# Optimization experiments

Measured on AMD Instinct MI355X. Metric: run time of the kernel, lower is better.

## Reference

```python
import jax, jax.numpy as jnp
import numpy as np

N_MODELS = 16
IN_F = 1024
OUT_F = 1024
N_TOK = 8192


def setup_inputs() -> dict:
    key = jax.random.key(0)
    k1, k2, k3, k4 = jax.random.split(key, 4)
    x = jax.random.normal(k1, (N_TOK, IN_F), dtype=jnp.float32)
    idxs = jax.random.randint(k2, (N_TOK,), 0, N_MODELS, dtype=jnp.int64)
    w = jax.random.normal(k3, (N_MODELS, IN_F, OUT_F), dtype=jnp.float32) * 0.02
    b = jax.random.normal(k4, (N_MODELS, OUT_F), dtype=jnp.float32) * 0.02
    return {"x": x, "idxs": idxs, "w": w, "b": b}


def reference(x, idxs, w, b):
    # Equivalent math to the torch loop: for each expert i, tokens with
    # idxs==i get x @ w[i] + b[i]; finally ReLU over all outputs.
    # Loop over the small fixed expert count; selection by mask avoids
    # materializing the [N, E, out] tensor or gathering per-token weights.
    y = jnp.zeros((x.shape[0], w.shape[2]), dtype=x.dtype)
    for i in range(w.shape[0]):
        yi = x @ w[i] + b[i]  # [N, out]
        y = jnp.where((idxs == i)[:, None], yi, y)
    return jax.nn.relu(y)
```

## Files before the change

### kernel.cpp

```cpp
#include <hip/hip_runtime.h>
#include <hip/hip_bf16.h>
#include <stdint.h>

#define N_MODELS 16
#define IN_F 1024
#define OUT_F 1024
#define N_TOK 8192
#define MAX_MT 80

typedef unsigned short u16;
using us4   = __attribute__((ext_vector_type(4))) unsigned short;
using s16x8 = __attribute__((ext_vector_type(8))) short;
using f32x4 = __attribute__((ext_vector_type(4))) float;

__device__ __forceinline__ u16 f2bf(float f) {
    union { float f; uint32_t u; } v;
    v.f = f;
    uint32_t u = v.u;
    u += 0x7fffu + ((u >> 16) & 1u);
    return (u16)(u >> 16);
}

__device__ __forceinline__ void gload16(const u16* g, u16* l) {
    __builtin_amdgcn_global_load_lds(
        (const __attribute__((address_space(1))) void*)g,
        (__attribute__((address_space(3))) void*)l, 16, 0, 0);
}

#define ROW 17
__global__ __launch_bounds__(256)
void setup_kernel(const int* __restrict__ idxs,
                  int* __restrict__ perm,
                  int* __restrict__ offs,
                  int* __restrict__ tile_off)
{
    __shared__ int cnt[256 * ROW];
    __shared__ int offsS[N_MODELS + 1];
    int t = threadIdx.x;

#pragma unroll
    for (int e = 0; e < N_MODELS; ++e) cnt[t * ROW + e] = 0;
    __syncthreads();

    int base = t * 32;
#pragma unroll
    for (int i = 0; i < 32; ++i) {
        int e = idxs[base + i];
        cnt[t * ROW + e] += 1;
    }
    __syncthreads();

#pragma unroll
    for (int s = 1; s < 256; s <<= 1) {
        int v[N_MODELS];
#pragma unroll
        for (int e = 0; e < N_MODELS; ++e)
            v[e] = (t >= s) ? cnt[(t - s) * ROW + e] : 0;
        __syncthreads();
#pragma unroll
        for (int e = 0; e < N_MODELS; ++e)
            cnt[t * ROW + e] += v[e];
        __syncthreads();
    }

    if (t == 0) {
        int o = 0, to = 0;
        for (int e = 0; e < N_MODELS; ++e) {
            int c = cnt[255 * ROW + e];
            offsS[e] = o;
            offs[e] = o; tile_off[e] = to;
            to += (c + 127) >> 7;
            o  += c;
        }
        offsS[N_MODELS] = o;
        offs[N_MODELS] = o; tile_off[N_MODELS] = to;
    }
    __syncthreads();

    int cur[N_MODELS];
#pragma unroll
    for (int e = 0; e < N_MODELS; ++e)
        cur[e] = offsS[e] + ((t > 0) ? cnt[(t - 1) * ROW + e] : 0);
    __syncthreads();
#pragma unroll
    for (int e = 0; e < N_MODELS; ++e) cnt[t * ROW + e] = cur[e];

#pragma unroll
    for (int i = 0; i < 32; ++i) {
        int tok = base + i;
        int e = idxs[tok];
        int p = cnt[t * ROW + e]++;
        perm[p] = tok;
    }
}

#define WBLOCKS (16 * 8 * 16)
#define XBLOCKS (MAX_MT * 8)

__global__ __launch_bounds__(256)
void prep_kernel(const float* __restrict__ w, const float* __restrict__ x,
                 const int* __restrict__ perm, const int* __restrict__ offs,
                 const int* __restrict__ tile_off,
                 u16* __restrict__ wT, u16* __restrict__ xg)
{
    int t  = threadIdx.x;
    int bx = blockIdx.x;

    if (bx < WBLOCKS) {
        int e   = bx >> 7;
        int nt  = (bx >> 4) & 7;
        int kb2 = bx & 15;
        const float* wp = w + (size_t)e * (IN_F * OUT_F) + (size_t)kb2 * 64 * OUT_F + nt * 128;
        u16* ob = wT + ((size_t)(e * 8 + nt) * 32 + kb2 * 2) * 4096;
        int n    = t & 127;
        int half = t >> 7;
#pragma unroll
        for (int i = 0; i < 4; ++i) {
            int ko = half + i * 2;
            s16x8 v;
#pragma unroll
            for (int j = 0; j < 8; ++j)
                v[j] = (short)f2bf(wp[(size_t)(ko * 8 + j) * OUT_F + n]);
            *(s16x8*)(ob + ((size_t)((ko >> 2) * 4 + (ko & 3)) * 128 + n) * 8) = v;
        }
    } else {
        __shared__ u16 sh[4096];
        int bx2 = bx - WBLOCKS;
        int mt  = bx2 >> 3;
        int kg  = bx2 & 7;
        int total = tile_off[N_MODELS];
        if (mt >= total) return;
        int e = 0;
        while (tile_off[e + 1] <= mt) ++e;
        int s0   = offs[e] + (mt - tile_off[e]) * 128;
        int sEnd = offs[e + 1];
        int r0   = t >> 3;
        int apos = t & 7;
        int toks[4];
#pragma unroll
        for (int i = 0; i < 4; ++i) {
            int r = r0 + i * 32;
            toks[i] = (s0 + r < sEnd) ? perm[s0 + r] : -1;
        }
        u16* outx = xg + (size_t)mt * 32 * 4096;
        for (int kb4 = 0; kb4 < 4; ++kb4) {
            int kb = kg * 4 + kb4;
#pragma unroll
            for (int i = 0; i < 4; ++i) {
                int r = r0 + i * 32;
                int k = kb * 32 + apos * 4;
                float4 v;
                if (toks[i] >= 0) v = *(const float4*)(x + (size_t)toks[i] * IN_F + k);
                else              v = make_float4(0.f, 0.f, 0.f, 0.f);
                us4 pk; pk.x = f2bf(v.x); pk.y = f2bf(v.y); pk.z = f2bf(v.z); pk.w = f2bf(v.w);
                *(us4*)(&sh[(apos >> 1) * 1024 + r * 8 + (apos & 1) * 4]) = pk;
            }
            __syncthreads();
#pragma unroll
            for (int i = 0; i < 2; ++i) {
                int c = t + i * 256;
                *(s16x8*)(outx + (size_t)kb * 4096 + c * 8) = *(const s16x8*)(&sh[c * 8]);
            }
            __syncthreads();
        }
    }
}

__global__ __launch_bounds__(256)
void gemm_kernel(const u16* __restrict__ xg, const u16* __restrict__ wT,
                 const float* __restrict__ bias,
                 const int* __restrict__ perm, const int* __restrict__ offs,
                 const int* __restrict__ tile_off,
                 float* __restrict__ out)
{
    __shared__ u16 As[4096];
    __shared__ u16 Bs[4096];
    __shared__ int   permS[128];
    __shared__ float biasS[128];
    __shared__ int   toS[N_MODELS + 1];

    int t  = threadIdx.x;
    int bt = blockIdx.y;
    int nt = blockIdx.x;

    if (t <= N_MODELS) toS[t] = tile_off[t];
    __syncthreads();
    if (bt >= toS[N_MODELS]) return;

    int e = 0;
    while (toS[e + 1] <= bt) ++e;
    int s0   = offs[e] + (bt - toS[e]) * 128;
    int sEnd = offs[e + 1];
    int mValid = sEnd - s0; if (mValid > 128) mValid = 128;

    if (t < 128) {
        permS[t] = (s0 + t < sEnd) ? perm[s0 + t] : 0;
        biasS[t] = bias[(size_t)e * OUT_F + nt * 128 + t];
    }

    const u16* atile = xg + (size_t)bt * 32 * 4096;
    const u16* btile = wT + ((size_t)(e * 8 + nt) * 32) * 4096;

    int lane = t & 63;
    int wv   = t >> 6;
    int wm   = (wv >> 1) * 64;
    int wn   = (wv & 1) * 64;
    int m    = lane & 15;
    int q    = lane >> 4;

    f32x4 acc[4][4];
#pragma unroll
    for (int i = 0; i < 4; ++i)
#pragma unroll
        for (int j = 0; j < 4; ++j)
            acc[i][j] = (f32x4){0.f, 0.f, 0.f, 0.f};

    int c = wv * 2;

    for (int kb = 0; kb < 32; ++kb) {
        const u16* ga = atile + kb * 4096;
        const u16* gb = btile + kb * 4096;
        gload16(ga + (c    ) * 512 + lane * 8, &As[(c    ) * 512]);
        gload16(ga + (c + 1) * 512 + lane * 8, &As[(c + 1) * 512]);
        gload16(gb + (c    ) * 512 + lane * 8, &Bs[(c    ) * 512]);
        gload16(gb + (c + 1) * 512 + lane * 8, &Bs[(c + 1) * 512]);
        __syncthreads();

        s16x8 af[4], bf[4];
#pragma unroll
        for (int mt2 = 0; mt2 < 4; ++mt2)
            af[mt2] = *(const s16x8*)(&As[q * 1024 + (wm + mt2 * 16 + m) * 8]);
#pragma unroll
        for (int nt2 = 0; nt2 < 4; ++nt2)
            bf[nt2] = *(const s16x8*)(&Bs[q * 1024 + (wn + nt2 * 16 + m) * 8]);
#pragma unroll
        for (int mt2 = 0; mt2 < 4; ++mt2)
#pragma unroll
            for (int nt2 = 0; nt2 < 4; ++nt2)
                acc[mt2][nt2] = __builtin_amdgcn_mfma_f32_16x16x32_bf16(
                    af[mt2], bf[nt2], acc[mt2][nt2], 0, 0, 0);
        __syncthreads();
    }

#pragma unroll
    for (int mt2 = 0; mt2 < 4; ++mt2) {
        int rbase = wm + mt2 * 16 + q * 4;
#pragma unroll
        for (int i = 0; i < 4; ++i) {
            int r = rbase + i;
            if (r < mValid) {
                int tok = permS[r];
                float* orow = out + (size_t)tok * OUT_F + nt * 128;
#pragma unroll
                for (int nt2 = 0; nt2 < 4; ++nt2) {
                    int col = wn + nt2 * 16 + m;
                    float v = acc[mt2][nt2][i] + biasS[col];
                    orow[col] = v > 0.f ? v : 0.f;
                }
            }
        }
    }
}

extern "C" void kernel_launch(void* const* d_in, const int* in_sizes, int n_in,
                              void* d_out, int out_size, void* d_ws, size_t ws_size,
                              hipStream_t stream) {
    const float* x    = (const float*)d_in[0];
    const int*   idxs = (const int*)d_in[1];
    const float* w    = (const float*)d_in[2];
    const float* b    = (const float*)d_in[3];
    float* out = (float*)d_out;

    u16* wT = (u16*)d_ws;
    u16* xg = wT + (size_t)N_MODELS * IN_F * OUT_F;
    int* perm     = (int*)(xg + (size_t)MAX_MT * 32 * 4096);
    int* offs     = perm + N_TOK;
    int* tile_off = offs + (N_MODELS + 1);

    setup_kernel<<<1, 256, 0, stream>>>(idxs, perm, offs, tile_off);
    prep_kernel<<<WBLOCKS + XBLOCKS, 256, 0, stream>>>(w, x, perm, offs, tile_off, wT, xg);
    gemm_kernel<<<dim3(8, MAX_MT), 256, 0, stream>>>(xg, wT, b, perm, offs, tile_off, out);
}
```

Baseline: 186.3 us.

## Fuse token gather and bf16 conversion into GEMM, merge routing into weight prep

Removes the separate x gather/convert pass and its intermediate bf16 buffer. The GEMM now loads fp32 rows of x directly through the permutation and converts them to bf16 in LDS each k-step. The routing setup becomes one extra block of the weight-conversion kernel, dropping a launch. In exchange, the GEMM re-reads fp32 x once per N-tile (8x) through uncoalesced, synchronous loads instead of async global-to-LDS copies.

```diff
diff --git a/kernel.cpp b/kernel.cpp
--- a/kernel.cpp
+++ b/kernel.cpp
@@ -27,82 +27,16 @@
         (__attribute__((address_space(3))) void*)l, 16, 0, 0);
 }
 
+#define WBLOCKS (16 * 8 * 16)
 #define ROW 17
+
 __global__ __launch_bounds__(256)
-void setup_kernel(const int* __restrict__ idxs,
-                  int* __restrict__ perm,
-                  int* __restrict__ offs,
-                  int* __restrict__ tile_off)
+void prep_kernel(const float* __restrict__ w, const int* __restrict__ idxs,
+                 u16* __restrict__ wT,
+                 int* __restrict__ perm, int* __restrict__ offs,
+                 int* __restrict__ tile_off)
 {
-    __shared__ int cnt[256 * ROW];
-    __shared__ int offsS[N_MODELS + 1];
-    int t = threadIdx.x;
-
-#pragma unroll
-    for (int e = 0; e < N_MODELS; ++e) cnt[t * ROW + e] = 0;
-    __syncthreads();
-
-    int base = t * 32;
-#pragma unroll
-    for (int i = 0; i < 32; ++i) {
-        int e = idxs[base + i];
-        cnt[t * ROW + e] += 1;
-    }
-    __syncthreads();
-
-#pragma unroll
-    for (int s = 1; s < 256; s <<= 1) {
-        int v[N_MODELS];
-#pragma unroll
-        for (int e = 0; e < N_MODELS; ++e)
-            v[e] = (t >= s) ? cnt[(t - s) * ROW + e] : 0;
-        __syncthreads();
-#pragma unroll
-        for (int e = 0; e < N_MODELS; ++e)
-            cnt[t * ROW + e] += v[e];
-        __syncthreads();
-    }
-
-    if (t == 0) {
-        int o = 0, to = 0;
-        for (int e = 0; e < N_MODELS; ++e) {
-            int c = cnt[255 * ROW + e];
-            offsS[e] = o;
-            offs[e] = o; tile_off[e] = to;
-            to += (c + 127) >> 7;
-            o  += c;
-        }
-        offsS[N_MODELS] = o;
-        offs[N_MODELS] = o; tile_off[N_MODELS] = to;
-    }
-    __syncthreads();
-
-    int cur[N_MODELS];
-#pragma unroll
-    for (int e = 0; e < N_MODELS; ++e)
-        cur[e] = offsS[e] + ((t > 0) ? cnt[(t - 1) * ROW + e] : 0);
-    __syncthreads();
-#pragma unroll
-    for (int e = 0; e < N_MODELS; ++e) cnt[t * ROW + e] = cur[e];
-
-#pragma unroll
-    for (int i = 0; i < 32; ++i) {
-        int tok = base + i;
-        int e = idxs[tok];
-        int p = cnt[t * ROW + e]++;
-        perm[p] = tok;
-    }
-}
-
-#define WBLOCKS (16 * 8 * 16)
-#define XBLOCKS (MAX_MT * 8)
-
-__global__ __launch_bounds__(256)
-void prep_kernel(const float* __restrict__ w, const float* __restrict__ x,
-                 const int* __restrict__ perm, const int* __restrict__ offs,
-                 const int* __restrict__ tile_off,
-                 u16* __restrict__ wT, u16* __restrict__ xg)
-{
+    __shared__ int shmem[256 * ROW + N_MODELS + 1];
     int t  = threadIdx.x;
     int bx = blockIdx.x;
 
@@ -110,64 +44,79 @@
         int e   = bx >> 7;
         int nt  = (bx >> 4) & 7;
         int kb2 = bx & 15;
-        const float* wp = w + (size_t)e * (IN_F * OUT_F) + (size_t)kb2 * 64 * OUT_F + nt * 128;
-        u16* ob = wT + ((size_t)(e * 8 + nt) * 32 + kb2 * 2) * 4096;
         int n    = t & 127;
         int half = t >> 7;
+        const float* wp = w + (size_t)e * (IN_F * OUT_F) + (size_t)kb2 * 64 * OUT_F + nt * 128 + n;
+        u16* ob = wT + ((size_t)(e * 8 + nt) * 32 + kb2 * 2) * 4096;
+        float r[32];
+#pragma unroll
+        for (int i = 0; i < 4; ++i) {
+            int ko = half + i * 2;
+#pragma unroll
+            for (int j = 0; j < 8; ++j)
+                r[i * 8 + j] = wp[(size_t)(ko * 8 + j) * OUT_F];
+        }
 #pragma unroll
         for (int i = 0; i < 4; ++i) {
             int ko = half + i * 2;
             s16x8 v;
 #pragma unroll
-            for (int j = 0; j < 8; ++j)
-                v[j] = (short)f2bf(wp[(size_t)(ko * 8 + j) * OUT_F + n]);
+            for (int j = 0; j < 8; ++j) v[j] = (short)f2bf(r[i * 8 + j]);
             *(s16x8*)(ob + ((size_t)((ko >> 2) * 4 + (ko & 3)) * 128 + n) * 8) = v;
         }
     } else {
-        __shared__ u16 sh[4096];
-        int bx2 = bx - WBLOCKS;
-        int mt  = bx2 >> 3;
-        int kg  = bx2 & 7;
-        int total = tile_off[N_MODELS];
-        if (mt >= total) return;
-        int e = 0;
-        while (tile_off[e + 1] <= mt) ++e;
-        int s0   = offs[e] + (mt - tile_off[e]) * 128;
-        int sEnd = offs[e + 1];
-        int r0   = t >> 3;
-        int apos = t & 7;
-        int toks[4];
-#pragma unroll
-        for (int i = 0; i < 4; ++i) {
-            int r = r0 + i * 32;
-            toks[i] = (s0 + r < sEnd) ? perm[s0 + r] : -1;
-        }
-        u16* outx = xg + (size_t)mt * 32 * 4096;
-        for (int kb4 = 0; kb4 < 4; ++kb4) {
-            int kb = kg * 4 + kb4;
-#pragma unroll
-            for (int i = 0; i < 4; ++i) {
-                int r = r0 + i * 32;
-                int k = kb * 32 + apos * 4;
-                float4 v;
-                if (toks[i] >= 0) v = *(const float4*)(x + (size_t)toks[i] * IN_F + k);
-                else              v = make_float4(0.f, 0.f, 0.f, 0.f);
-                us4 pk; pk.x = f2bf(v.x); pk.y = f2bf(v.y); pk.z = f2bf(v.z); pk.w = f2bf(v.w);
-                *(us4*)(&sh[(apos >> 1) * 1024 + r * 8 + (apos & 1) * 4]) = pk;
+        int* cnt   = shmem;
+        int* offsS = shmem + 256 * ROW;
+#pragma unroll
+        for (int e = 0; e < N_MODELS; ++e) cnt[t * ROW + e] = 0;
+        __syncthreads();
+        int base = t * 32;
+#pragma unroll
+        for (int i = 0; i < 32; ++i) cnt[t * ROW + idxs[base + i]] += 1;
+        __syncthreads();
+#pragma unroll
+        for (int s = 1; s < 256; s <<= 1) {
+            int v[N_MODELS];
+#pragma unroll
+            for (int e = 0; e < N_MODELS; ++e)
+                v[e] = (t >= s) ? cnt[(t - s) * ROW + e] : 0;
+            __syncthreads();
+#pragma unroll
+            for (int e = 0; e < N_MODELS; ++e)
+                cnt[t * ROW + e] += v[e];
+            __syncthreads();
+        }
+        if (t == 0) {
+            int o = 0, to = 0;
+            for (int e = 0; e < N_MODELS; ++e) {
+                int c = cnt[255 * ROW + e];
+                offsS[e] = o;
+                offs[e] = o; tile_off[e] = to;
+                to += (c + 127) >> 7;
+                o  += c;
             }
-            __syncthreads();
-#pragma unroll
-            for (int i = 0; i < 2; ++i) {
-                int c = t + i * 256;
-                *(s16x8*)(outx + (size_t)kb * 4096 + c * 8) = *(const s16x8*)(&sh[c * 8]);
-            }
-            __syncthreads();
+            offsS[N_MODELS] = o;
+            offs[N_MODELS] = o; tile_off[N_MODELS] = to;
+        }
+        __syncthreads();
+        int cur[N_MODELS];
+#pragma unroll
+        for (int e = 0; e < N_MODELS; ++e)
+            cur[e] = offsS[e] + ((t > 0) ? cnt[(t - 1) * ROW + e] : 0);
+        __syncthreads();
+#pragma unroll
+        for (int e = 0; e < N_MODELS; ++e) cnt[t * ROW + e] = cur[e];
+#pragma unroll
+        for (int i = 0; i < 32; ++i) {
+            int tok = base + i;
+            int e = idxs[tok];
+            perm[cnt[t * ROW + e]++] = tok;
         }
     }
 }
 
 __global__ __launch_bounds__(256)
-void gemm_kernel(const u16* __restrict__ xg, const u16* __restrict__ wT,
+void gemm_kernel(const float* __restrict__ x, const u16* __restrict__ wT,
                  const float* __restrict__ bias,
                  const int* __restrict__ perm, const int* __restrict__ offs,
                  const int* __restrict__ tile_off,
@@ -197,8 +146,19 @@
         permS[t] = (s0 + t < sEnd) ? perm[s0 + t] : 0;
         biasS[t] = bias[(size_t)e * OUT_F + nt * 128 + t];
     }
-
-    const u16* atile = xg + (size_t)bt * 32 * 4096;
+    __syncthreads();
+
+    const float* px[4];
+    int la[4];
+#pragma unroll
+    for (int i = 0; i < 4; ++i) {
+        int c    = t + i * 256;
+        int r    = c >> 3;
+        int apos = c & 7;
+        px[i] = x + (size_t)permS[r] * IN_F + apos * 4;
+        la[i] = (apos >> 1) * 1024 + r * 8 + (apos & 1) * 4;
+    }
+
     const u16* btile = wT + ((size_t)(e * 8 + nt) * 32) * 4096;
 
     int lane = t & 63;
@@ -215,15 +175,22 @@
         for (int j = 0; j < 4; ++j)
             acc[i][j] = (f32x4){0.f, 0.f, 0.f, 0.f};
 
-    int c = wv * 2;
+    int c2 = wv * 2;
 
     for (int kb = 0; kb < 32; ++kb) {
-        const u16* ga = atile + kb * 4096;
         const u16* gb = btile + kb * 4096;
-        gload16(ga + (c    ) * 512 + lane * 8, &As[(c    ) * 512]);
-        gload16(ga + (c + 1) * 512 + lane * 8, &As[(c + 1) * 512]);
-        gload16(gb + (c    ) * 512 + lane * 8, &Bs[(c    ) * 512]);
-        gload16(gb + (c + 1) * 512 + lane * 8, &Bs[(c + 1) * 512]);
+        gload16(gb + (c2    ) * 512 + lane * 8, &Bs[(c2    ) * 512]);
+        gload16(gb + (c2 + 1) * 512 + lane * 8, &Bs[(c2 + 1) * 512]);
+#pragma unroll
+        for (int i = 0; i < 4; ++i) {
+            const float4 v = *(const float4*)(px[i] + kb * 32);
+            union { __hip_bfloat162 h; uint32_t u; } lo, hi;
+            lo.h = __float22bfloat162_rn(make_float2(v.x, v.y));
+            hi.h = __float22bfloat162_rn(make_float2(v.z, v.w));
+            union { us4 s; uint32_t u[2]; } pk;
+            pk.u[0] = lo.u; pk.u[1] = hi.u;
+            *(us4*)(&As[la[i]]) = pk.s;
+        }
         __syncthreads();
 
         s16x8 af[4], bf[4];
@@ -272,12 +239,10 @@
     float* out = (float*)d_out;
 
     u16* wT = (u16*)d_ws;
-    u16* xg = wT + (size_t)N_MODELS * IN_F * OUT_F;
-    int* perm     = (int*)(xg + (size_t)MAX_MT * 32 * 4096);
+    int* perm     = (int*)(wT + (size_t)N_MODELS * IN_F * OUT_F);
     int* offs     = perm + N_TOK;
     int* tile_off = offs + (N_MODELS + 1);
 
-    setup_kernel<<<1, 256, 0, stream>>>(idxs, perm, offs, tile_off);
-    prep_kernel<<<WBLOCKS + XBLOCKS, 256, 0, stream>>>(w, x, perm, offs, tile_off, wT, xg);
-    gemm_kernel<<<dim3(8, MAX_MT), 256, 0, stream>>>(xg, wT, b, perm, offs, tile_off, out);
-}
+    prep_kernel<<<WBLOCKS + 1, 256, 0, stream>>>(w, idxs, wT, perm, offs, tile_off);
+    gemm_kernel<<<dim3(8, MAX_MT), 256, 0, stream>>>(x, wT, b, perm, offs, tile_off, out);
+}
```

Result: slower. 190.5 us (+2.3%).
